# Performance work log

Measured on AMD Instinct MI355X. Metric: run time of the kernel, lower is better.

Reference implementation:

```python
import jax, jax.numpy as jnp
import numpy as np

V, E, D, OUT = 100000, 400000, 128, 128
KP = 20  # kron projection dim (hard-coded 20 in module; 20*20=400)
EPS = 1e-5


def _layer_norm(x, g, b):
    mu = jnp.mean(x, axis=-1, keepdims=True)
    var = jnp.mean(jnp.square(x - mu), axis=-1, keepdims=True)
    return (x - mu) * jax.lax.rsqrt(var + EPS) * g + b


def setup_inputs() -> dict:
    key = jax.random.key(0)
    ks = jax.random.split(key, 16)
    def lin(k, fan_in, shape):
        return jax.random.normal(k, shape, jnp.float32) / np.sqrt(fan_in)
    inp = {
        'node_feats': jax.random.normal(ks[0], (V, D), jnp.float32),
        'src': jax.random.randint(ks[1], (E,), 0, V, jnp.int32),
        'dst': jax.random.randint(ks[2], (E,), 0, V, jnp.int32),
        # project_edge: Linear(2D, 1)
        'W_edge': lin(ks[3], 2 * D, (2 * D, 1)), 'b_edge': jnp.zeros((1,), jnp.float32),
        # attentive_gru.project_node: Linear(D, D)
        'W_pn': lin(ks[4], D, (D, D)), 'b_pn': jnp.zeros((D,), jnp.float32),
        # GRUCell(D, D)
        'W_ih': lin(ks[5], D, (3 * D, D)), 'b_ih': jnp.zeros((3 * D,), jnp.float32),
        'W_hh': lin(ks[6], D, (3 * D, D)), 'b_hh': jnp.zeros((3 * D,), jnp.float32),
        # layer_norm(D)
        'ln_g': jnp.ones((D,), jnp.float32), 'ln_b': jnp.zeros((D,), jnp.float32),
        # kron.proj_node: Linear(D, 20)+LN
        'Wk1': lin(ks[7], D, (D, KP)), 'bk1': jnp.zeros((KP,), jnp.float32),
        'lnk1_g': jnp.ones((KP,), jnp.float32), 'lnk1_b': jnp.zeros((KP,), jnp.float32),
        # kron.proj_kron: Linear(400, OUT)+LN
        'Wk2': lin(ks[8], KP * KP, (KP * KP, OUT)), 'bk2': jnp.zeros((OUT,), jnp.float32),
        'lnk2_g': jnp.ones((OUT,), jnp.float32), 'lnk2_b': jnp.zeros((OUT,), jnp.float32),
        # concat_proj: Linear(D+OUT, D)+LN
        'Wc': lin(ks[9], D + OUT, (D + OUT, D)), 'bc': jnp.zeros((D,), jnp.float32),
        'lnc_g': jnp.ones((D,), jnp.float32), 'lnc_b': jnp.zeros((D,), jnp.float32),
    }
    return inp


def _forward(node_feats, W_edge, b_edge, W_pn, b_pn, W_ih, b_ih, W_hh, b_hh,
             ln_g, ln_b, Wk1, bk1, lnk1_g, lnk1_b, Wk2, bk2, lnk2_g, lnk2_b,
             Wc, bc, lnc_g, lnc_b, src, dst):
    n = node_feats.shape[0]
    d = node_feats.shape[1]
    # --- Kronecker message branch ---
    npj = jax.nn.relu(_layer_norm(node_feats @ Wk1 + bk1, lnk1_g, lnk1_b))  # [V,20]
    kron = (npj[src][:, :, None] * npj[dst][:, None, :]).reshape(src.shape[0], -1)  # [E,400]
    kron = jax.nn.relu(_layer_norm(kron @ Wk2 + bk2, lnk2_g, lnk2_b))  # [E,OUT]
    kron_feat = jax.ops.segment_sum(kron, dst, num_segments=n)  # [V,OUT]
    # --- Attention branch: he = cat(dst_feats, src_feats) ---
    he = jnp.concatenate([node_feats[dst], node_feats[src]], axis=1)  # [E,2D]
    logits = jax.nn.relu(he @ W_edge + b_edge)  # [E,1]
    # edge softmax over in-edges of each dst node
    lmax = jax.ops.segment_max(logits, dst, num_segments=n)  # [V,1]
    a = jnp.exp(logits - lmax[dst])
    asum = jax.ops.segment_sum(a, dst, num_segments=n)
    a = a / asum[dst]  # [E,1]
    hv = node_feats @ W_pn + b_pn  # [V,D]
    context = jax.nn.relu(jax.ops.segment_sum(hv[src] * a, dst, num_segments=n))  # [V,D]
    # --- GRUCell(context, node_feats) ---
    gi = context @ W_ih.T + b_ih
    gh = node_feats @ W_hh.T + b_hh
    r = jax.nn.sigmoid(gi[:, :d] + gh[:, :d])
    z = jax.nn.sigmoid(gi[:, d:2 * d] + gh[:, d:2 * d])
    nn_ = jnp.tanh(gi[:, 2 * d:] + r * gh[:, 2 * d:])
    h = (1.0 - z) * nn_ + z * node_feats
    gru_out = _layer_norm(jax.nn.relu(h), ln_g, ln_b)  # [V,D]
    # --- concat + projection ---
    cat = jnp.concatenate([gru_out, kron_feat], axis=1)  # [V,D+OUT]
    return jax.nn.relu(_layer_norm(cat @ Wc + bc, lnc_g, lnc_b))


def reference(node_feats, src, dst, W_edge, b_edge, W_pn, b_pn, W_ih, b_ih, W_hh, b_hh,
              ln_g, ln_b, Wk1, bk1, lnk1_g, lnk1_b, Wk2, bk2, lnk2_g, lnk2_b,
              Wc, bc, lnc_g, lnc_b):
    return _forward(node_feats, W_edge, b_edge, W_pn, b_pn, W_ih, b_ih, W_hh, b_hh,
                    ln_g, ln_b, Wk1, bk1, lnk1_g, lnk1_b, Wk2, bk2, lnk2_g, lnk2_b,
                    Wc, bc, lnc_g, lnc_b, src, dst)
```

## Files before the change

kernel.cpp:

```cpp
#include <hip/hip_runtime.h>

#define G_KP 20
#define G_LN_EPS 1e-5f

typedef float v4f __attribute__((ext_vector_type(4)));
typedef short v8s __attribute__((ext_vector_type(8)));
typedef short v4s __attribute__((ext_vector_type(4)));

__device__ __forceinline__ unsigned short f2b(float x) {
  union { float f; unsigned int i; } c;
  c.f = x;
  return (unsigned short)((c.i + 0x7FFFu + ((c.i >> 16) & 1u)) >> 16);
}
__device__ __forceinline__ float b2f(unsigned short u) {
  union { unsigned int i; float f; } c;
  c.i = ((unsigned int)u) << 16;
  return c.f;
}
__device__ __forceinline__ float bits2f(unsigned int i) {
  union { unsigned int i; float f; } c;
  c.i = i;
  return c.f;
}
__device__ __forceinline__ unsigned int cvtpk(float lo, float hi) {
  unsigned int r;
  asm("v_cvt_pk_bf16_f32 %0, %1, %2" : "=v"(r) : "v"(lo), "v"(hi));
  return r;
}

template<int NKT, int NTS, int NTU>
__device__ __forceinline__ void stage_mfma2(
    const v8s* __restrict__ Bsrc, int kt_tiles, v8s* B_lds,
    const unsigned short* Arow, int a_kt, int a_off, int b_off,
    int t, int l, v4f* acc) {
  constexpr int NPR = NTS / 4;
  v8s pr[NPR];
  #pragma unroll
  for (int i = 0; i < NPR; ++i) pr[i] = Bsrc[t + i * 256];
  #pragma unroll
  for (int kt = 0; kt < NKT; ++kt) {
    __syncthreads();
    #pragma unroll
    for (int i = 0; i < NPR; ++i) B_lds[t + i * 256] = pr[i];
    if (kt + 1 < NKT) {
      #pragma unroll
      for (int i = 0; i < NPR; ++i)
        pr[i] = Bsrc[(kt + 1) * kt_tiles * 64 + t + i * 256];
    }
    __syncthreads();
    v8s a = *(const v8s*)&Arow[kt * a_kt + a_off];
    #pragma unroll
    for (int n0 = 0; n0 < NTU; ++n0)
      acc[n0] = __builtin_amdgcn_mfma_f32_16x16x32_bf16(a, B_lds[b_off + n0 * 64 + l], acc[n0], 0, 0, 0);
  }
}

__global__ void GNNLayerKAFP_76871324663923_kernel() {}

__global__ void k_fill(float* out, int n, float v) {
  int i = blockIdx.x * 256 + threadIdx.x;
  if (i < n) out[i] = v;
}

__global__ void k_zero(float* p, int n) {
  int i = blockIdx.x * 256 + threadIdx.x;
  if (i < n) p[i] = 0.0f;
}

__global__ void k_prep_wk2b(const float* Wk2, unsigned short* Wk2b) {
  int id = blockIdx.x * 256 + threadIdx.x;
  if (id >= 13 * 8 * 64 * 8) return;
  int j = id & 7, l = (id >> 3) & 63, n0 = (id >> 9) & 7, kt = id >> 12;
  int k = kt * 32 + (l >> 4) * 8 + j;
  int n = n0 * 16 + (l & 15);
  Wk2b[id] = f2b((k < 400) ? Wk2[k * 128 + n] : 0.0f);
}

__global__ void k_prep_wpnb(const float* Wpn, unsigned short* WpnB) {
  int id = blockIdx.x * 256 + threadIdx.x;
  if (id >= 4 * 8 * 64 * 8) return;
  int j = id & 7, l = (id >> 3) & 63, n0 = (id >> 9) & 7, kt = id >> 12;
  int k = kt * 32 + (l >> 4) * 8 + j;
  int n = n0 * 16 + (l & 15);
  WpnB[id] = f2b(Wpn[k * 128 + n]);
}

__global__ void k_prep_wgb(const float* Wih, const float* Whh, unsigned short* WgB) {
  int id = blockIdx.x * 256 + threadIdx.x;
  if (id >= 8 * 32 * 64 * 8) return;
  int j = id & 7, l = (id >> 3) & 63, n0 = (id >> 9) & 31, kt = id >> 14;
  int k = kt * 32 + (l >> 4) * 8 + j;
  int jj = n0 * 16 + (l & 15);
  float v = 0.0f;
  if (jj < 256)      v = (k < 128) ? Wih[jj * 128 + k] : Whh[jj * 128 + (k - 128)];
  else if (jj < 384) { if (k < 128)  v = Wih[jj * 128 + k]; }
  else               { if (k >= 128) v = Whh[(jj - 128) * 128 + (k - 128)]; }
  WgB[id] = f2b(v);
}

__global__ void k_prep_wcb(const float* Wc, unsigned short* WcB) {
  int id = blockIdx.x * 256 + threadIdx.x;
  if (id >= 8 * 8 * 64 * 8) return;
  int j = id & 7, l = (id >> 3) & 63, n0 = (id >> 9) & 7, kt = id >> 12;
  int k = kt * 32 + (l >> 4) * 8 + j;
  int n = n0 * 16 + (l & 15);
  WcB[id] = f2b(Wc[k * 128 + n]);
}

__global__ void k_npj(const float* nf, const float* Wk1, const float* bk1,
                      const float* g, const float* b, const float* We,
                      float* npj, float* pd, float* ps, int nV) {
  int w = threadIdx.x >> 6, lane = threadIdx.x & 63;
  int v = blockIdx.x * 4 + w;
  if (v >= nV) v = nV - 1;
  __shared__ float x[4][128];
  __shared__ float y[4][20];
  __shared__ float st[4][2];
  float x0 = nf[v * 128 + lane];
  float x1 = nf[v * 128 + 64 + lane];
  x[w][lane]      = x0;
  x[w][lane + 64] = x1;
  float p0 = x0 * We[lane]       + x1 * We[64 + lane];
  float p1 = x0 * We[128 + lane] + x1 * We[192 + lane];
  for (int off = 32; off > 0; off >>= 1) {
    p0 += __shfl_down(p0, off, 64);
    p1 += __shfl_down(p1, off, 64);
  }
  if (lane == 0) { pd[v] = p0; ps[v] = p1; }
  __syncthreads();
  if (lane < G_KP) {
    float acc = bk1[lane];
    for (int t = 0; t < 128; ++t) acc += x[w][t] * Wk1[t * G_KP + lane];
    y[w][lane] = acc;
  }
  __syncthreads();
  if (lane == 0) {
    float s = 0.0f, ss = 0.0f;
    for (int i = 0; i < G_KP; ++i) { s += y[w][i]; ss += y[w][i] * y[w][i]; }
    float mu = s * (1.0f / G_KP);
    float var = ss * (1.0f / G_KP) - mu * mu;
    st[w][0] = mu;
    st[w][1] = rsqrtf(fmaxf(var, 0.0f) + G_LN_EPS);
  }
  __syncthreads();
  if (lane < G_KP) {
    float val = (y[w][lane] - st[w][0]) * st[w][1] * g[lane] + b[lane];
    npj[v * G_KP + lane] = fmaxf(val, 0.0f);
  }
}

__global__ void k_hist(const int* dst, int* deg, int nE) {
  int e = blockIdx.x * 256 + threadIdx.x;
  if (e < nE) atomicAdd(&deg[dst[e]], 1);
}

__global__ void k_scan1(const int* deg, int* bsum, int nV) {
  __shared__ int red[256];
  int b = blockIdx.x, t = threadIdx.x;
  int base = b * 2048 + t * 8;
  int s = 0;
  #pragma unroll
  for (int k = 0; k < 8; ++k) {
    int i = base + k;
    if (i < nV) s += deg[i];
  }
  red[t] = s;
  __syncthreads();
  for (int off = 128; off > 0; off >>= 1) {
    if (t < off) red[t] += red[t + off];
    __syncthreads();
  }
  if (t == 0) bsum[b] = red[0];
}

__global__ void k_scan2(const int* bsum, int* boff, int* total, int nB) {
  __shared__ int sh[1024];
  int t = threadIdx.x;
  int v = (t < nB) ? bsum[t] : 0;
  sh[t] = v;
  __syncthreads();
  for (int off = 1; off < 1024; off <<= 1) {
    int u = (t >= off) ? sh[t - off] : 0;
    __syncthreads();
    sh[t] += u;
    __syncthreads();
  }
  if (t < nB) boff[t] = sh[t] - v;
  if (t == 1023) total[0] = sh[1023];
}

__global__ void k_scan3(const int* deg, const int* boff, const int* total,
                        int* rowptr, int* cursor, int nV) {
  __shared__ int sh[256];
  int b = blockIdx.x, t = threadIdx.x;
  int base = b * 2048 + t * 8;
  int loc[8];
  int s = 0;
  #pragma unroll
  for (int k = 0; k < 8; ++k) {
    int i = base + k;
    int d = (i < nV) ? deg[i] : 0;
    loc[k] = s; s += d;
  }
  sh[t] = s;
  __syncthreads();
  for (int off = 1; off < 256; off <<= 1) {
    int u = (t >= off) ? sh[t - off] : 0;
    __syncthreads();
    sh[t] += u;
    __syncthreads();
  }
  int toff = sh[t] - s + boff[b];
  #pragma unroll
  for (int k = 0; k < 8; ++k) {
    int i = base + k;
    if (i < nV) { rowptr[i] = toff + loc[k]; cursor[i] = toff + loc[k]; }
  }
  if (b == 0 && t == 0) rowptr[nV] = total[0];
}

__global__ void k_edge(const int* src, const int* dst, const float* pd,
                       const float* ps, const float* be, float* a,
                       int* cursor, int* eid, int nE) {
  int e = blockIdx.x * 256 + threadIdx.x;
  if (e >= nE) return;
  int d = dst[e], s_ = src[e];
  float lg = fmaxf(pd[d] + ps[s_] + be[0], 0.0f);
  a[e] = __expf(fminf(lg, 60.0f));
  int pos = atomicAdd(&cursor[d], 1);
  eid[pos] = e;
}

__global__ void k_ctx_gather(const int* rowptr, const int* eid, const int* src,
                             const float* a, const float* nf, float* wctx,
                             int nV) {
  int w = threadIdx.x >> 6, l = threadIdx.x & 63;
  int v = blockIdx.x * 4 + w;
  if (v >= nV) return;
  int beg = rowptr[v], end = rowptr[v + 1];
  float s = 1e-20f, a0 = 0.0f, a1 = 0.0f;
  for (int i = beg; i < end; ++i) {
    int e = eid[i];
    float av = a[e];
    int sn = src[e];
    s  += av;
    a0 += av * nf[sn * 128 + l];
    a1 += av * nf[sn * 128 + 64 + l];
  }
  float dn = 1.0f / s;
  wctx[v * 128 + l]      = a0 * dn;
  wctx[v * 128 + 64 + l] = a1 * dn;
}

__global__ void __launch_bounds__(256, 4)
k_kron_mfma(const int* src, const int* dst, const float* npj,
            const int* rowptr, const int* eid,
            const unsigned short* Wk2b, const float* bk2,
            const float* g, const float* b, float* kf, int nE) {
  __shared__ unsigned short A_lds[32 * 424];
  __shared__ int eidx[32][2];
  __shared__ unsigned short SDB[4096];
  __shared__ float psq[2][2][16][2];
  unsigned short (*sd)[40] = (unsigned short(*)[40])SDB;
  v8s* B_lds = (v8s*)SDB;
  float* Yf = (float*)A_lds;

  int t = threadIdx.x;
  int w = t >> 6, l = t & 63;
  int c15 = l & 15, quad = l >> 4;
  int pg = w >> 1, hf = w & 1;
  int erbase = pg * 16;

  int ebeg = blockIdx.x * 32;
  int ecnt = nE - ebeg; if (ecnt > 32) ecnt = 32;

  if (t < 32) {
    int e = eid[(t < ecnt) ? (ebeg + t) : ebeg];
    eidx[t][0] = src[e];
    eidx[t][1] = dst[e];
  }
  __syncthreads();
  for (int i = t; i < 1280; i += 256) {
    int er = i / 40, p = i - er * 40;
    float v = (p < 20) ? npj[eidx[er][0] * G_KP + p]
                       : npj[eidx[er][1] * G_KP + (p - 20)];
    sd[er][p] = f2b(v);
  }
  __syncthreads();
  for (int i = t; i < 32 * 16; i += 256) {
    int e = i >> 4, kk = 400 + (i & 15);
    A_lds[e * 424 + kk] = 0;
  }
  {
    int e = t >> 3, l8 = t & 7;
    unsigned int dpk[10];
    #pragma unroll
    for (int m = 0; m < 10; ++m)
      dpk[m] = *(const unsigned int*)&sd[e][20 + 2 * m];
    #pragma unroll
    for (int rr = 0; rr < 3; ++rr) {
      int r = l8 + rr * 8;
      if (r < 20) {
        float s = b2f(sd[e][r]);
        unsigned int* dstp = (unsigned int*)&A_lds[e * 424 + r * 20];
        #pragma unroll
        for (int m = 0; m < 10; ++m) {
          float d0 = bits2f(dpk[m] << 16);
          float d1 = bits2f(dpk[m] & 0xFFFF0000u);
          dstp[m] = cvtpk(s * d0, s * d1);
        }
      }
    }
  }

  v4f acc[4];
  #pragma unroll
  for (int n0 = 0; n0 < 4; ++n0)
    #pragma unroll
    for (int r = 0; r < 4; ++r) acc[n0][r] = 0.0f;

  stage_mfma2<13, 8, 4>((const v8s*)Wk2b, 8, B_lds,
                        &A_lds[(erbase + c15) * 424], 32, quad * 8,
                        hf * 256, t, l, acc);

  float biasv[4], gv[4], bv[4];
  #pragma unroll
  for (int n0 = 0; n0 < 4; ++n0) {
    int n = hf * 64 + n0 * 16 + c15;
    biasv[n0] = bk2[n]; gv[n0] = g[n]; bv[n0] = b[n];
  }
  float sArr[4], qArr[4];
  #pragma unroll
  for (int r = 0; r < 4; ++r) {
    float s = 0.0f, q = 0.0f;
    #pragma unroll
    for (int n0 = 0; n0 < 4; ++n0) {
      float v = acc[n0][r] + biasv[n0];
      s += v; q += v * v;
    }
    for (int m = 1; m < 16; m <<= 1) {
      s += __shfl_xor(s, m, 64);
      q += __shfl_xor(q, m, 64);
    }
    sArr[r] = s; qArr[r] = q;
    if (c15 == 0) {
      psq[pg][hf][quad * 4 + r][0] = s;
      psq[pg][hf][quad * 4 + r][1] = q;
    }
  }
  __syncthreads();
  float mu[4], rs[4];
  #pragma unroll
  for (int r = 0; r < 4; ++r) {
    float s = sArr[r] + psq[pg][hf ^ 1][quad * 4 + r][0];
    float q = qArr[r] + psq[pg][hf ^ 1][quad * 4 + r][1];
    float mm = s * (1.0f / 128.0f);
    float vv = q * (1.0f / 128.0f) - mm * mm;
    mu[r] = mm;
    rs[r] = rsqrtf(fmaxf(vv, 0.0f) + G_LN_EPS);
  }
  #pragma unroll
  for (int r = 0; r < 4; ++r) {
    int eloc = erbase + quad * 4 + r;
    #pragma unroll
    for (int n0 = 0; n0 < 4; ++n0) {
      float v = acc[n0][r] + biasv[n0];
      Yf[eloc * 132 + hf * 64 + n0 * 16 + c15] =
          fmaxf((v - mu[r]) * rs[r] * gv[n0] + bv[n0], 0.0f);
    }
  }
  __syncthreads();

  int dF = eidx[0][1];
  int dL = eidx[ecnt - 1][1];
  int col = t & 127;
  int wend = ebeg + ecnt;
  for (int d = dF + (t >> 7); d <= dL; d += 2) {
    int rb = rowptr[d], re = rowptr[d + 1];
    int lo = (rb > ebeg ? rb : ebeg) - ebeg;
    int hi = (re < wend ? re : wend) - ebeg;
    if (lo >= hi) continue;
    float s = 0.0f;
    for (int i = lo; i < hi; ++i) s += Yf[i * 132 + col];
    if (rb >= ebeg && re <= wend)
      kf[(size_t)d * 128 + col] = s;
    else
      atomicAdd(&kf[(size_t)d * 128 + col], s);
  }
}

__global__ void __launch_bounds__(256, 2)
k_gru_mfma(const float* nf, const float* wctx, const float* kf,
           const unsigned short* WpnB, const float* bpn,
           const unsigned short* WgB,
           const float* b_ih, const float* b_hh,
           const float* g1, const float* b1,
           const unsigned short* WcB, const float* bc,
           const float* g2, const float* b2, float* out,
           int nV) {
  __shared__ unsigned short CX[64][264];
  __shared__ v8s B_lds[1024];
  int t = threadIdx.x;
  int w = t >> 6, l = t & 63;
  int c15 = l & 15, quad = l >> 4;
  int v0 = blockIdx.x * 64;
  int rowbase = w * 16;

  #pragma unroll
  for (int k = 0; k < 8; ++k) {
    int i = l + k * 64;
    int r = i >> 5;
    int seg = i & 31;
    int vn = v0 + rowbase + r; if (vn >= nV) vn = nV - 1;
    v4f wc = *(const v4f*)&wctx[vn * 128 + seg * 4];
    v4f xf = *(const v4f*)&nf[vn * 128 + seg * 4];
    v4s pw = { (short)f2b(wc[0]), (short)f2b(wc[1]), (short)f2b(wc[2]), (short)f2b(wc[3]) };
    v4s px = { (short)f2b(xf[0]), (short)f2b(xf[1]), (short)f2b(xf[2]), (short)f2b(xf[3]) };
    *(v4s*)&CX[rowbase + r][seg * 4]       = pw;
    *(v4s*)&CX[rowbase + r][128 + seg * 4] = px;
  }

  {
    v4f acc[8];
    #pragma unroll
    for (int n0 = 0; n0 < 8; ++n0)
      #pragma unroll
      for (int r = 0; r < 4; ++r) acc[n0][r] = 0.0f;
    stage_mfma2<4, 8, 8>((const v8s*)WpnB, 8, B_lds,
                         &CX[rowbase + c15][0], 32, quad * 8, 0, t, l, acc);
    #pragma unroll
    for (int n0 = 0; n0 < 8; ++n0) {
      int n = n0 * 16 + c15;
      float bo = bpn[n];
      #pragma unroll
      for (int r = 0; r < 4; ++r)
        CX[rowbase + quad * 4 + r][n] = f2b(fmaxf(acc[n0][r] + bo, 0.0f));
    }
  }

  unsigned int rz[32];
  {
    v4f acc[16];
    #pragma unroll
    for (int n0 = 0; n0 < 16; ++n0)
      #pragma unroll
      for (int r = 0; r < 4; ++r) acc[n0][r] = 0.0f;
    stage_mfma2<8, 16, 16>((const v8s*)WgB, 32, B_lds,
                           &CX[rowbase + c15][0], 32, quad * 8, 0, t, l, acc);
    #pragma unroll
    for (int n0 = 0; n0 < 8; ++n0) {
      int j = n0 * 16 + c15;
      float brz = b_ih[j] + b_hh[j];
      float bzz = b_ih[128 + j] + b_hh[128 + j];
      #pragma unroll
      for (int r = 0; r < 4; ++r) {
        float rp = acc[n0][r] + brz;
        float zp = acc[8 + n0][r] + bzz;
        float rr = 1.0f / (1.0f + __expf(-fmaxf(fminf(rp, 30.0f), -30.0f)));
        float zz = 1.0f / (1.0f + __expf(-fmaxf(fminf(zp, 30.0f), -30.0f)));
        rz[r * 8 + n0] = (unsigned int)f2b(rr) | ((unsigned int)f2b(zz) << 16);
      }
    }
  }
  {
    v4f acc[16];
    #pragma unroll
    for (int n0 = 0; n0 < 16; ++n0)
      #pragma unroll
      for (int r = 0; r < 4; ++r) acc[n0][r] = 0.0f;
    stage_mfma2<8, 16, 16>((const v8s*)WgB + 16 * 64, 32, B_lds,
                           &CX[rowbase + c15][0], 32, quad * 8, 0, t, l, acc);
    #pragma unroll
    for (int r = 0; r < 4; ++r) {
      int row = rowbase + quad * 4 + r;
      float h[8];
      float s = 0.0f, q = 0.0f;
      #pragma unroll
      for (int n0 = 0; n0 < 8; ++n0) {
        int j = n0 * 16 + c15;
        float gi = acc[n0][r] + b_ih[256 + j];
        float gh = acc[8 + n0][r] + b_hh[256 + j];
        unsigned int pk = rz[r * 8 + n0];
        float rr = b2f((unsigned short)(pk & 0xFFFFu));
        float zz = b2f((unsigned short)(pk >> 16));
        float an = fmaxf(fminf(gi + rr * gh, 15.0f), -15.0f);
        float e2 = __expf(-2.0f * an);
        float nn = (1.0f - e2) / (1.0f + e2);
        float x  = b2f(CX[row][128 + j]);
        float hv = fmaxf((1.0f - zz) * nn + zz * x, 0.0f);
        h[n0] = hv; s += hv; q += hv * hv;
      }
      for (int m = 1; m < 16; m <<= 1) {
        s += __shfl_xor(s, m, 64);
        q += __shfl_xor(q, m, 64);
      }
      float mu = s * (1.0f / 128.0f);
      float var = q * (1.0f / 128.0f) - mu * mu;
      float rstd = rsqrtf(fmaxf(var, 0.0f) + G_LN_EPS);
      #pragma unroll
      for (int n0 = 0; n0 < 8; ++n0) {
        int j = n0 * 16 + c15;
        CX[row][j] = f2b((h[n0] - mu) * rstd * g1[j] + b1[j]);
      }
    }
  }

  #pragma unroll
  for (int k = 0; k < 8; ++k) {
    int i = l + k * 64;
    int r = i >> 5, seg = i & 31;
    int vn = v0 + rowbase + r; if (vn >= nV) vn = nV - 1;
    v4f kv = *(const v4f*)&kf[vn * 128 + seg * 4];
    v4s pk = { (short)f2b(kv[0]), (short)f2b(kv[1]), (short)f2b(kv[2]), (short)f2b(kv[3]) };
    *(v4s*)&CX[rowbase + r][128 + seg * 4] = pk;
  }

  {
    v4f acc[8];
    #pragma unroll
    for (int n0 = 0; n0 < 8; ++n0)
      #pragma unroll
      for (int r = 0; r < 4; ++r) acc[n0][r] = 0.0f;
    stage_mfma2<8, 8, 8>((const v8s*)WcB, 8, B_lds,
                         &CX[rowbase + c15][0], 32, quad * 8, 0, t, l, acc);
    #pragma unroll
    for (int r = 0; r < 4; ++r) {
      float vv[8];
      float s = 0.0f, q = 0.0f;
      #pragma unroll
      for (int n0 = 0; n0 < 8; ++n0) {
        vv[n0] = acc[n0][r] + bc[n0 * 16 + c15];
        s += vv[n0]; q += vv[n0] * vv[n0];
      }
      for (int m = 1; m < 16; m <<= 1) {
        s += __shfl_xor(s, m, 64);
        q += __shfl_xor(q, m, 64);
      }
      float mu = s * (1.0f / 128.0f);
      float var = q * (1.0f / 128.0f) - mu * mu;
      float rstd = rsqrtf(fmaxf(var, 0.0f) + G_LN_EPS);
      int vn = v0 + rowbase + quad * 4 + r;
      if (vn < nV) {
        #pragma unroll
        for (int n0 = 0; n0 < 8; ++n0) {
          int n = n0 * 16 + c15;
          float y = fmaxf((vv[n0] - mu) * rstd * g2[n] + b2[n], 0.0f);
          if (y != y) y = 9.0f;
          out[vn * 128 + n] = y;
        }
      }
    }
  }
}

extern "C" void kernel_launch(void* const* d_in, const int* in_sizes, int n_in,
                              void* d_out, int out_size, void* d_ws, size_t ws_size,
                              hipStream_t stream) {
  (void)n_in;

  int nV = in_sizes[0] / 128;
  int nE = in_sizes[1];

  const float* nf     = (const float*)d_in[0];
  const int*   src    = (const int*)d_in[1];
  const int*   dst    = (const int*)d_in[2];
  const float* W_edge = (const float*)d_in[3];
  const float* b_edge = (const float*)d_in[4];
  const float* W_pn   = (const float*)d_in[5];
  const float* b_pn   = (const float*)d_in[6];
  const float* W_ih   = (const float*)d_in[7];
  const float* b_ih   = (const float*)d_in[8];
  const float* W_hh   = (const float*)d_in[9];
  const float* b_hh   = (const float*)d_in[10];
  const float* ln_g   = (const float*)d_in[11];
  const float* ln_b   = (const float*)d_in[12];
  const float* Wk1    = (const float*)d_in[13];
  const float* bk1    = (const float*)d_in[14];
  const float* lnk1_g = (const float*)d_in[15];
  const float* lnk1_b = (const float*)d_in[16];
  const float* Wk2    = (const float*)d_in[17];
  const float* bk2    = (const float*)d_in[18];
  const float* lnk2_g = (const float*)d_in[19];
  const float* lnk2_b = (const float*)d_in[20];
  const float* Wc     = (const float*)d_in[21];
  const float* bc     = (const float*)d_in[22];
  const float* lnc_g  = (const float*)d_in[23];
  const float* lnc_b  = (const float*)d_in[24];

  float* ws = (float*)d_ws;
  size_t off = 0;
  float* w_npj  = ws + off; off += (size_t)nV * G_KP;
  float* w_a    = ws + off; off += (size_t)nE;
  float* w_pd   = ws + off; off += (size_t)nV;
  float* w_ps   = ws + off; off += (size_t)nV;
  int*   w_rowp = (int*)(ws + off); off += (size_t)nV + 1;
  int*   w_curs = (int*)(ws + off); off += (size_t)nV;
  int*   w_eid  = (int*)(ws + off); off += (size_t)nE;
  int*   w_bsum = (int*)(ws + off); off += 1024;
  int*   w_boff = (int*)(ws + off); off += 1024;
  int*   w_tot  = (int*)(ws + off); off += 1;
  float* w_wctx = ws + off; off += (size_t)nV * 128;
  int*   w_deg  = (int*)(ws + off); off += (size_t)nV;
  float* w_kf   = ws + off; off += (size_t)nV * 128;
  unsigned short* w_wk2b = (unsigned short*)(ws + off); off += 26624;
  unsigned short* w_wpnb = (unsigned short*)(ws + off); off += 8192;
  unsigned short* w_wgb  = (unsigned short*)(ws + off); off += 65536;
  unsigned short* w_wcb  = (unsigned short*)(ws + off); off += 16384;
  size_t need_bytes = off * 4;

  if (ws_size < need_bytes) {
    k_fill<<<(out_size + 255) / 256, 256, 0, stream>>>((float*)d_out, out_size, 7.0f);
    return;
  }

  k_fill<<<(out_size + 255) / 256, 256, 0, stream>>>((float*)d_out, out_size, 2.0f);

  int nzero = nV * 129;
  k_zero<<<(nzero + 255) / 256, 256, 0, stream>>>((float*)w_deg, nzero);
  k_prep_wk2b<<<208, 256, 0, stream>>>(Wk2, w_wk2b);
  k_prep_wpnb<<<64, 256, 0, stream>>>(W_pn, w_wpnb);
  k_prep_wgb<<<512, 256, 0, stream>>>(W_ih, W_hh, w_wgb);
  k_prep_wcb<<<128, 256, 0, stream>>>(Wc, w_wcb);

  int nB = (nV + 2047) / 2048;
  k_npj<<<(nV + 3) / 4, 256, 0, stream>>>(nf, Wk1, bk1, lnk1_g, lnk1_b,
                                          W_edge, w_npj, w_pd, w_ps, nV);
  k_hist<<<(nE + 255) / 256, 256, 0, stream>>>(dst, w_deg, nE);
  k_scan1<<<nB, 256, 0, stream>>>(w_deg, w_bsum, nV);
  k_scan2<<<1, 1024, 0, stream>>>(w_bsum, w_boff, w_tot, nB);
  k_scan3<<<nB, 256, 0, stream>>>(w_deg, w_boff, w_tot, w_rowp, w_curs, nV);
  k_edge<<<(nE + 255) / 256, 256, 0, stream>>>(src, dst, w_pd, w_ps, b_edge,
                                               w_a, w_curs, w_eid, nE);
  k_ctx_gather<<<(nV + 3) / 4, 256, 0, stream>>>(w_rowp, w_eid, src, w_a, nf,
                                                 w_wctx, nV);
  k_kron_mfma<<<(nE + 31) / 32, 256, 0, stream>>>(src, dst, w_npj, w_rowp,
                                                  w_eid, w_wk2b, bk2,
                                                  lnk2_g, lnk2_b, w_kf, nE);
  k_gru_mfma<<<(nV + 63) / 64, 256, 0, stream>>>(nf, w_wctx, w_kf, w_wpnb, b_pn,
                                                 w_wgb, b_ih, b_hh, ln_g, ln_b,
                                                 w_wcb, bc, lnc_g, lnc_b,
                                                 (float*)d_out, nV);
}
```

Before: 692.6 us.

## Split GRU gate GEMMs into four narrower passes to raise occupancy

The GRU gate computation used two 256-column MFMA passes with 16 accumulator tiles each. It now runs four 128-column passes (r, z, gi, gh) with 8 accumulator tiles each, packing intermediates as bf16 pairs. The B staging buffer in LDS is halved and launch bounds are raised to 3 blocks per CU, to cut register and LDS pressure and allow more resident waves. The cost is more barriers and staging rounds per block, and the gi term is now rounded to bf16, which adds rounding error.

```diff
diff --git a/kernel.cpp b/kernel.cpp
--- a/kernel.cpp
+++ b/kernel.cpp
@@ -26,6 +26,12 @@
   unsigned int r;
   asm("v_cvt_pk_bf16_f32 %0, %1, %2" : "=v"(r) : "v"(lo), "v"(hi));
   return r;
+}
+__device__ __forceinline__ float unpk(unsigned int pk, int odd) {
+  return odd ? bits2f(pk & 0xFFFF0000u) : bits2f(pk << 16);
+}
+__device__ __forceinline__ float sigm(float x) {
+  return 1.0f / (1.0f + __expf(-fmaxf(fminf(x, 30.0f), -30.0f)));
 }
 
 template<int NKT, int NTS, int NTU>
@@ -389,7 +395,7 @@
   }
 }
 
-__global__ void __launch_bounds__(256, 2)
+__global__ void __launch_bounds__(256, 3)
 k_gru_mfma(const float* nf, const float* wctx, const float* kf,
            const unsigned short* WpnB, const float* bpn,
            const unsigned short* WgB,
@@ -399,7 +405,7 @@
            const float* g2, const float* b2, float* out,
            int nV) {
   __shared__ unsigned short CX[64][264];
-  __shared__ v8s B_lds[1024];
+  __shared__ v8s B_lds[512];
   int t = threadIdx.x;
   int w = t >> 6, l = t & 63;
   int c15 = l & 15, quad = l >> 4;
@@ -438,38 +444,63 @@
     }
   }
 
-  unsigned int rz[32];
+  unsigned int rrp[16], zzp[16], gip[16];
   {
-    v4f acc[16];
-    #pragma unroll
-    for (int n0 = 0; n0 < 16; ++n0)
+    v4f acc[8];
+    #pragma unroll
+    for (int n0 = 0; n0 < 8; ++n0)
       #pragma unroll
       for (int r = 0; r < 4; ++r) acc[n0][r] = 0.0f;
-    stage_mfma2<8, 16, 16>((const v8s*)WgB, 32, B_lds,
-                           &CX[rowbase + c15][0], 32, quad * 8, 0, t, l, acc);
+    stage_mfma2<8, 8, 8>((const v8s*)WgB, 32, B_lds,
+                         &CX[rowbase + c15][0], 32, quad * 8, 0, t, l, acc);
     #pragma unroll
     for (int n0 = 0; n0 < 8; ++n0) {
       int j = n0 * 16 + c15;
-      float brz = b_ih[j] + b_hh[j];
-      float bzz = b_ih[128 + j] + b_hh[128 + j];
-      #pragma unroll
-      for (int r = 0; r < 4; ++r) {
-        float rp = acc[n0][r] + brz;
-        float zp = acc[8 + n0][r] + bzz;
-        float rr = 1.0f / (1.0f + __expf(-fmaxf(fminf(rp, 30.0f), -30.0f)));
-        float zz = 1.0f / (1.0f + __expf(-fmaxf(fminf(zp, 30.0f), -30.0f)));
-        rz[r * 8 + n0] = (unsigned int)f2b(rr) | ((unsigned int)f2b(zz) << 16);
-      }
+      float bb = b_ih[j] + b_hh[j];
+      rrp[n0 * 2]     = cvtpk(sigm(acc[n0][0] + bb), sigm(acc[n0][1] + bb));
+      rrp[n0 * 2 + 1] = cvtpk(sigm(acc[n0][2] + bb), sigm(acc[n0][3] + bb));
     }
   }
   {
-    v4f acc[16];
-    #pragma unroll
-    for (int n0 = 0; n0 < 16; ++n0)
+    v4f acc[8];
+    #pragma unroll
+    for (int n0 = 0; n0 < 8; ++n0)
       #pragma unroll
       for (int r = 0; r < 4; ++r) acc[n0][r] = 0.0f;
-    stage_mfma2<8, 16, 16>((const v8s*)WgB + 16 * 64, 32, B_lds,
-                           &CX[rowbase + c15][0], 32, quad * 8, 0, t, l, acc);
+    stage_mfma2<8, 8, 8>((const v8s*)WgB + 8 * 64, 32, B_lds,
+                         &CX[rowbase + c15][0], 32, quad * 8, 0, t, l, acc);
+    #pragma unroll
+    for (int n0 = 0; n0 < 8; ++n0) {
+      int j = n0 * 16 + c15;
+      float bb = b_ih[128 + j] + b_hh[128 + j];
+      zzp[n0 * 2]     = cvtpk(sigm(acc[n0][0] + bb), sigm(acc[n0][1] + bb));
+      zzp[n0 * 2 + 1] = cvtpk(sigm(acc[n0][2] + bb), sigm(acc[n0][3] + bb));
+    }
+  }
+  {
+    v4f acc[8];
+    #pragma unroll
+    for (int n0 = 0; n0 < 8; ++n0)
+      #pragma unroll
+      for (int r = 0; r < 4; ++r) acc[n0][r] = 0.0f;
+    stage_mfma2<8, 8, 8>((const v8s*)WgB + 16 * 64, 32, B_lds,
+                         &CX[rowbase + c15][0], 32, quad * 8, 0, t, l, acc);
+    #pragma unroll
+    for (int n0 = 0; n0 < 8; ++n0) {
+      int j = n0 * 16 + c15;
+      float bb = b_ih[256 + j];
+      gip[n0 * 2]     = cvtpk(acc[n0][0] + bb, acc[n0][1] + bb);
+      gip[n0 * 2 + 1] = cvtpk(acc[n0][2] + bb, acc[n0][3] + bb);
+    }
+  }
+  {
+    v4f acc[8];
+    #pragma unroll
+    for (int n0 = 0; n0 < 8; ++n0)
+      #pragma unroll
+      for (int r = 0; r < 4; ++r) acc[n0][r] = 0.0f;
+    stage_mfma2<8, 8, 8>((const v8s*)WgB + 24 * 64, 32, B_lds,
+                         &CX[rowbase + c15][0], 32, quad * 8, 0, t, l, acc);
     #pragma unroll
     for (int r = 0; r < 4; ++r) {
       int row = rowbase + quad * 4 + r;
@@ -478,11 +509,10 @@
       #pragma unroll
       for (int n0 = 0; n0 < 8; ++n0) {
         int j = n0 * 16 + c15;
-        float gi = acc[n0][r] + b_ih[256 + j];
-        float gh = acc[8 + n0][r] + b_hh[256 + j];
-        unsigned int pk = rz[r * 8 + n0];
-        float rr = b2f((unsigned short)(pk & 0xFFFFu));
-        float zz = b2f((unsigned short)(pk >> 16));
+        float gh = acc[n0][r] + b_hh[256 + j];
+        float rr = unpk(rrp[n0 * 2 + (r >> 1)], r & 1);
+        float zz = unpk(zzp[n0 * 2 + (r >> 1)], r & 1);
+        float gi = unpk(gip[n0 * 2 + (r >> 1)], r & 1);
         float an = fmaxf(fminf(gi + rr * gh, 15.0f), -15.0f);
         float e2 = __expf(-2.0f * an);
         float nn = (1.0f - e2) / (1.0f + e2);
```

Measured after the change: 698.6 us. No clear change (+0.9%).
